# Performance work log

Hardware: AMD Instinct MI355X
Metric: run time of the kernel (lower is better)

The kernel has to match this reference:

```python
import jax, jax.numpy as jnp
import numpy as np

BS, T, IN, HS = 512, 2048, 64, 128


def setup_inputs() -> dict:
    key = jax.random.key(0)
    ks = jax.random.split(key, 6)
    stdv = 1.0 / np.sqrt(HS)
    u = lambda k, shape: jax.random.uniform(k, shape, jnp.float32, -stdv, stdv)
    return {
        "x": jax.random.normal(ks[0], (BS, T, IN), jnp.float32),
        "W": u(ks[1], (IN, 4 * HS)),
        "U": u(ks[2], (HS, 4 * HS)),
        "bias": u(ks[3], (4 * HS,)),
        "linear_w": u(ks[4], (1, HS)),
        "linear_b": u(ks[5], (1,)),
    }


def reference(x, W, U, bias, linear_w, linear_b):
    bs = x.shape[0]
    h0 = jnp.zeros((bs, HS), x.dtype)
    c0 = jnp.zeros((bs, HS), x.dtype)

    def step(carry, x_t):
        h, c = carry
        gates = x_t @ W + h @ U + bias  # [bs, 4*HS]
        i_t = jax.nn.sigmoid(gates[:, :HS])
        f_t = jax.nn.sigmoid(gates[:, HS:2 * HS])
        g_t = jnp.tanh(gates[:, 2 * HS:3 * HS])
        o_t = jax.nn.sigmoid(gates[:, 3 * HS:])
        c = f_t * c + i_t * g_t
        h = o_t * jnp.tanh(c)
        return (h, c), None

    xs = jnp.swapaxes(x, 0, 1)  # [T, bs, IN]
    (h_t, c_t), _ = jax.lax.scan(step, (h0, c0), xs)
    y_t = h_t @ linear_w.T + linear_b  # [bs, 1]
    return (y_t, h_t, c_t)
```

## Files before the change

kernel.cpp:

```cpp
#include <hip/hip_runtime.h>


#define T_STEPS 2048
#define IN_DIM 64
#define HS 128
#define NG 512
#define ROWS 2
#define NBLK 256
#define NTHR 512
#define CH 32
#define NCH (T_STEPS / CH)
#define HROW 144

typedef float f32x4 __attribute__((ext_vector_type(4)));
typedef short s16x8 __attribute__((ext_vector_type(8)));
typedef int   i32x4 __attribute__((ext_vector_type(4)));

__device__ __forceinline__ unsigned f2bf(float f) {
  unsigned u = __float_as_uint(f);
  return (u + 0x7fffu + ((u >> 16) & 1u)) >> 16;
}
__device__ __forceinline__ float bf2f(unsigned short s) {
  return __int_as_float(((int)s) << 16);
}
__device__ __forceinline__ float rcpf(float x) { return __builtin_amdgcn_rcpf(x); }
__device__ __forceinline__ float sigm(float x) { return rcpf(1.f + __expf(-x)); }
__device__ __forceinline__ float tanhfast(float x) {
  return 1.0f - 2.0f * rcpf(__expf(2.0f * x) + 1.0f);
}
__device__ __forceinline__ int xswz(int f) { return f ^ (((f >> 7) & 7) << 3); }

__global__ __launch_bounds__(NTHR, 1)
void lstm_fused(const float* __restrict__ X, const float* __restrict__ W,
                const float* __restrict__ U, const float* __restrict__ B,
                const float* __restrict__ LW, const float* __restrict__ LB,
                float* __restrict__ OUT) {
  __shared__ __align__(16) short Zc[CH * 128 * 8];
  __shared__ __align__(16) float Xl[4096];
  __shared__ __align__(16) unsigned char Hq[2][2][HROW];
  __shared__ float Ys[256];
  __shared__ float Ps[8];

  const int tid  = threadIdx.x;
  const int lane = tid & 63;
  const int w    = tid >> 6;
  const int blk  = blockIdx.x;
  const int lrow = lane & 15;
  const int lg   = lane >> 4;
  const int col8 = (w * 16 + lrow) * 8;

  i32x4 bUq[4][2];
  float scl[4];
  s16x8 bfrW[4][2];
  float biasg[4];
#pragma unroll
  for (int n = 0; n < 4; ++n) {
    const int p = n * HS + w * 16 + lrow;
    float m = 1e-8f;
    for (int k = 0; k < HS; ++k) m = fmaxf(m, fabsf(U[k * NG + p]));
    const float rsu = 127.f / m;
    scl[n] = m / (127.f * 127.f);
#pragma unroll
    for (int kt = 0; kt < 2; ++kt) {
      int vq[4] = {0, 0, 0, 0};
      for (int j = 0; j < 16; ++j) {
        const int k = kt * 64 + (lg << 4) + j;
        int q = (int)rintf(U[k * NG + p] * rsu);
        q = q < -127 ? -127 : (q > 127 ? 127 : q);
        vq[j >> 2] |= (q & 0xff) << ((j & 3) * 8);
      }
      bUq[n][kt] = (i32x4){vq[0], vq[1], vq[2], vq[3]};
    }
#pragma unroll
    for (int kt = 0; kt < 2; ++kt)
#pragma unroll
      for (int j = 0; j < 8; ++j)
        bfrW[n][kt][j] = (short)f2bf(W[(kt * 32 + (lg << 3) + j) * NG + p]);
    biasg[n] = B[p];
  }

  f32x4 sx0, sx1, sx2, sx3;
  auto stage_load = [&](int cc) {
    if (w < 4) {
#pragma unroll
      for (int q = 0; q < 4; ++q) {
        const int f   = w * 1024 + q * 256 + lane * 4;
        const int tlc = f >> 7;
        const int row = (f >> 6) & 1;
        const int k   = f & 63;
        const f32x4 v = *(const f32x4*)(
            X + ((long)(blk * ROWS + row) * T_STEPS + (long)cc * CH + tlc) * IN_DIM + k);
        if (q == 0) sx0 = v; else if (q == 1) sx1 = v;
        else if (q == 2) sx2 = v; else sx3 = v;
      }
    }
  };
  auto stage_write = [&]() {
    if (w < 4) {
#pragma unroll
      for (int q = 0; q < 4; ++q) {
        const int f = w * 1024 + q * 256 + lane * 4;
        const f32x4 v = (q == 0) ? sx0 : (q == 1) ? sx1 : (q == 2) ? sx2 : sx3;
        *(f32x4*)&Xl[xswz(f)] = v;
      }
    }
  };

  stage_load(0);
  stage_write();
  for (int i = tid; i < 2 * 2 * HROW; i += NTHR) ((unsigned char*)Hq)[i] = 0;

  i32x4 afr[2];
  const i32x4 izer = {0, 0, 0, 0};
  afr[0] = izer; afr[1] = izer;

  float creg = 0.f, hreg = 0.f;
  __syncthreads();

#pragma unroll 1
  for (int c = 0; c < NCH; ++c) {
#pragma unroll
    for (int mt = 0; mt < 4; ++mt) {
      const int fb = mt * 1024 + (lrow >> 1) * 128 + (lrow & 1) * 64;
      const int f0 = xswz(fb + 8 * lg);
      const int f1 = xswz(fb + 32 + 8 * lg);
      const f32x4 x0 = *(const f32x4*)&Xl[f0];
      const f32x4 x1 = *(const f32x4*)&Xl[f0 + 4];
      const f32x4 x2 = *(const f32x4*)&Xl[f1];
      const f32x4 x3 = *(const f32x4*)&Xl[f1 + 4];
      s16x8 a0, a1;
#pragma unroll
      for (int j = 0; j < 4; ++j) {
        a0[j] = (short)f2bf(x0[j]); a0[4 + j] = (short)f2bf(x1[j]);
        a1[j] = (short)f2bf(x2[j]); a1[4 + j] = (short)f2bf(x3[j]);
      }
      f32x4 ac[4];
#pragma unroll
      for (int n = 0; n < 4; ++n) {
        ac[n][0] = biasg[n]; ac[n][1] = biasg[n];
        ac[n][2] = biasg[n]; ac[n][3] = biasg[n];
      }
#pragma unroll
      for (int n = 0; n < 4; ++n)
        ac[n] = __builtin_amdgcn_mfma_f32_16x16x32_bf16(a0, bfrW[n][0], ac[n], 0, 0, 0);
#pragma unroll
      for (int n = 0; n < 4; ++n)
        ac[n] = __builtin_amdgcn_mfma_f32_16x16x32_bf16(a1, bfrW[n][1], ac[n], 0, 0, 0);
      s16x8 z0, z1;
#pragma unroll
      for (int n = 0; n < 4; ++n) {
        z0[n] = (short)f2bf(ac[n][0]); z0[4 + n] = (short)f2bf(ac[n][1]);
        z1[n] = (short)f2bf(ac[n][2]); z1[4 + n] = (short)f2bf(ac[n][3]);
      }
      const int tl0 = mt * 8 + 2 * lg;
      *(s16x8*)&Zc[tl0 * 1024 + col8]       = z0;
      *(s16x8*)&Zc[(tl0 + 1) * 1024 + col8] = z1;
    }
    __syncthreads();
    stage_load((c + 1 < NCH) ? c + 1 : c);

#pragma unroll 1
    for (int tl = 0; tl < CH; ++tl) {
      const int t = c * CH + tl;
      const uint2 zu = *(const uint2*)&Zc[tl * 1024 + col8 + (lg & 1) * 4];

      i32x4 acc[4];
#pragma unroll
      for (int n = 0; n < 4; ++n) acc[n] = izer;

      __builtin_amdgcn_s_setprio(1);
#pragma unroll
      for (int kt = 0; kt < 2; ++kt) {
        acc[0] = __builtin_amdgcn_mfma_i32_16x16x64_i8(afr[kt], bUq[0][kt], acc[0], 0, 0, 0);
        acc[1] = __builtin_amdgcn_mfma_i32_16x16x64_i8(afr[kt], bUq[1][kt], acc[1], 0, 0, 0);
        acc[2] = __builtin_amdgcn_mfma_i32_16x16x64_i8(afr[kt], bUq[2][kt], acc[2], 0, 0, 0);
        acc[3] = __builtin_amdgcn_mfma_i32_16x16x64_i8(afr[kt], bUq[3][kt], acc[3], 0, 0, 0);
      }
      __builtin_amdgcn_s_setprio(0);

      if (tl == 4) stage_write();

      if (lane < 32) {
        const float v0 = (float)acc[0][0] * scl[0] + bf2f((unsigned short)(zu.x & 0xffff));
        const float v1 = (float)acc[1][0] * scl[1] + bf2f((unsigned short)(zu.x >> 16));
        const float v2 = (float)acc[2][0] * scl[2] + bf2f((unsigned short)(zu.y & 0xffff));
        const float v3 = (float)acc[3][0] * scl[3] + bf2f((unsigned short)(zu.y >> 16));
        const float iv = sigm(v0), fv = sigm(v1);
        const float gv = tanhfast(v2), ov = sigm(v3);
        creg = fv * creg + iv * gv;
        hreg = ov * tanhfast(creg);
        const int colc = w * 16 + lrow;
        const int r    = lg;
        if (t < T_STEPS - 1) {
          const int hq = (int)rintf(hreg * 127.f);
          Hq[(t + 1) & 1][r][colc] = (unsigned char)hq;
        } else {
          const int row = blk * ROWS + r;
          OUT[512 + row * HS + colc]   = hreg;
          OUT[66048 + row * HS + colc] = creg;
          Ys[r * HS + colc] = LW[colc] * hreg;
        }
      }
      __syncthreads();

      if (t < T_STEPS - 1 && (lrow & 3) == 0 && lrow < 8) {
        const unsigned char* hb = Hq[(t + 1) & 1][lrow >> 2];
        afr[0] = *(const i32x4*)&hb[lg << 4];
        afr[1] = *(const i32x4*)&hb[64 + (lg << 4)];
      }
    }
  }

  if (tid < 8) {
    const int r = tid >> 2, seg = tid & 3;
    float s = 0.f;
#pragma unroll 8
    for (int j = 0; j < 32; ++j) s += Ys[r * 128 + seg * 32 + j];
    Ps[tid] = s;
  }
  __syncthreads();
  if (tid < ROWS) {
    OUT[blk * ROWS + tid] = LB[0] + Ps[tid * 4] + Ps[tid * 4 + 1]
                                  + Ps[tid * 4 + 2] + Ps[tid * 4 + 3];
  }
}

extern "C" void kernel_launch(void* const* d_in, const int* in_sizes, int n_in,
                              void* d_out, int out_size, void* d_ws, size_t ws_size,
                              hipStream_t stream) {
  const float* X  = (const float*)d_in[0];
  const float* W  = (const float*)d_in[1];
  const float* U  = (const float*)d_in[2];
  const float* B  = (const float*)d_in[3];
  const float* LW = (const float*)d_in[4];
  const float* LB = (const float*)d_in[5];
  lstm_fused<<<dim3(NBLK), dim3(NTHR), 0, stream>>>(X, W, U, B, LW, LB, (float*)d_out);
}
```

Measured before the change: 931.1 us.

## Skew two batch rows by half a step to overlap recurrence MFMA with gate math

Splits the two batch rows of each block into separately buffered pipelines, with row B lagging row A by one timestep phase. Row A's gate math now overlaps row B's int8 recurrence MFMAs, and the reverse, so the matrix and vector work of the serial chain can interleave. Each row gets its own h buffer and fragment registers, and an epilogue finishes row B's last step. This adds one more barrier per timestep and more registers in exchange for hiding the latency of the dependent chain.

Measured after the change: 1.699 ms. 1.83x slower.

```diff
diff --git a/kernel.cpp b/kernel.cpp
--- a/kernel.cpp
+++ b/kernel.cpp
@@ -37,7 +37,8 @@
                 float* __restrict__ OUT) {
   __shared__ __align__(16) short Zc[CH * 128 * 8];
   __shared__ __align__(16) float Xl[4096];
-  __shared__ __align__(16) unsigned char Hq[2][2][HROW];
+  __shared__ __align__(16) unsigned char HqA[HROW];
+  __shared__ __align__(16) unsigned char HqB[HROW];
   __shared__ float Ys[256];
   __shared__ float Ps[8];
 
@@ -108,12 +109,13 @@
 
   stage_load(0);
   stage_write();
-  for (int i = tid; i < 2 * 2 * HROW; i += NTHR) ((unsigned char*)Hq)[i] = 0;
-
-  i32x4 afr[2];
+  for (int i = tid; i < HROW; i += NTHR) { HqA[i] = 0; HqB[i] = 0; }
+
   const i32x4 izer = {0, 0, 0, 0};
-  afr[0] = izer; afr[1] = izer;
-
+  i32x4 afrA[2] = {izer, izer};
+  i32x4 afrB[2] = {izer, izer};
+  i32x4 accB[4] = {izer, izer, izer, izer};
+  uint2 zuB = {0u, 0u};
   float creg = 0.f, hreg = 0.f;
   __syncthreads();
 
@@ -164,52 +166,96 @@
       const int t = c * CH + tl;
       const uint2 zu = *(const uint2*)&Zc[tl * 1024 + col8 + (lg & 1) * 4];
 
-      i32x4 acc[4];
-#pragma unroll
-      for (int n = 0; n < 4; ++n) acc[n] = izer;
-
+      if (t > 0 && lg == 1) {
+        const float v0 = (float)accB[0][0] * scl[0] + bf2f((unsigned short)(zuB.x & 0xffff));
+        const float v1 = (float)accB[1][0] * scl[1] + bf2f((unsigned short)(zuB.x >> 16));
+        const float v2 = (float)accB[2][0] * scl[2] + bf2f((unsigned short)(zuB.y & 0xffff));
+        const float v3 = (float)accB[3][0] * scl[3] + bf2f((unsigned short)(zuB.y >> 16));
+        const float iv = sigm(v0), fv = sigm(v1);
+        const float gv = tanhfast(v2), ov = sigm(v3);
+        creg = fv * creg + iv * gv;
+        hreg = ov * tanhfast(creg);
+        HqB[w * 16 + lrow] = (unsigned char)(int)rintf(hreg * 127.f);
+      }
+      zuB = zu;
+
+      i32x4 accA[4] = {izer, izer, izer, izer};
       __builtin_amdgcn_s_setprio(1);
 #pragma unroll
       for (int kt = 0; kt < 2; ++kt) {
-        acc[0] = __builtin_amdgcn_mfma_i32_16x16x64_i8(afr[kt], bUq[0][kt], acc[0], 0, 0, 0);
-        acc[1] = __builtin_amdgcn_mfma_i32_16x16x64_i8(afr[kt], bUq[1][kt], acc[1], 0, 0, 0);
-        acc[2] = __builtin_amdgcn_mfma_i32_16x16x64_i8(afr[kt], bUq[2][kt], acc[2], 0, 0, 0);
-        acc[3] = __builtin_amdgcn_mfma_i32_16x16x64_i8(afr[kt], bUq[3][kt], acc[3], 0, 0, 0);
+        accA[0] = __builtin_amdgcn_mfma_i32_16x16x64_i8(afrA[kt], bUq[0][kt], accA[0], 0, 0, 0);
+        accA[1] = __builtin_amdgcn_mfma_i32_16x16x64_i8(afrA[kt], bUq[1][kt], accA[1], 0, 0, 0);
+        accA[2] = __builtin_amdgcn_mfma_i32_16x16x64_i8(afrA[kt], bUq[2][kt], accA[2], 0, 0, 0);
+        accA[3] = __builtin_amdgcn_mfma_i32_16x16x64_i8(afrA[kt], bUq[3][kt], accA[3], 0, 0, 0);
       }
       __builtin_amdgcn_s_setprio(0);
-
-      if (tl == 4) stage_write();
-
-      if (lane < 32) {
-        const float v0 = (float)acc[0][0] * scl[0] + bf2f((unsigned short)(zu.x & 0xffff));
-        const float v1 = (float)acc[1][0] * scl[1] + bf2f((unsigned short)(zu.x >> 16));
-        const float v2 = (float)acc[2][0] * scl[2] + bf2f((unsigned short)(zu.y & 0xffff));
-        const float v3 = (float)acc[3][0] * scl[3] + bf2f((unsigned short)(zu.y >> 16));
+      __syncthreads();
+
+      if (lrow == 4) {
+        afrB[0] = *(const i32x4*)&HqB[lg << 4];
+        afrB[1] = *(const i32x4*)&HqB[64 + (lg << 4)];
+      }
+
+      if (lg == 0) {
+        const float v0 = (float)accA[0][0] * scl[0] + bf2f((unsigned short)(zu.x & 0xffff));
+        const float v1 = (float)accA[1][0] * scl[1] + bf2f((unsigned short)(zu.x >> 16));
+        const float v2 = (float)accA[2][0] * scl[2] + bf2f((unsigned short)(zu.y & 0xffff));
+        const float v3 = (float)accA[3][0] * scl[3] + bf2f((unsigned short)(zu.y >> 16));
         const float iv = sigm(v0), fv = sigm(v1);
         const float gv = tanhfast(v2), ov = sigm(v3);
         creg = fv * creg + iv * gv;
         hreg = ov * tanhfast(creg);
         const int colc = w * 16 + lrow;
-        const int r    = lg;
         if (t < T_STEPS - 1) {
-          const int hq = (int)rintf(hreg * 127.f);
-          Hq[(t + 1) & 1][r][colc] = (unsigned char)hq;
+          HqA[colc] = (unsigned char)(int)rintf(hreg * 127.f);
         } else {
-          const int row = blk * ROWS + r;
+          const int row = blk * ROWS;
           OUT[512 + row * HS + colc]   = hreg;
           OUT[66048 + row * HS + colc] = creg;
-          Ys[r * HS + colc] = LW[colc] * hreg;
+          Ys[colc] = LW[colc] * hreg;
         }
       }
+
+      __builtin_amdgcn_s_setprio(1);
+#pragma unroll
+      for (int kt = 0; kt < 2; ++kt) {
+        accB[0] = (kt == 0) ? __builtin_amdgcn_mfma_i32_16x16x64_i8(afrB[0], bUq[0][0], izer, 0, 0, 0)
+                            : __builtin_amdgcn_mfma_i32_16x16x64_i8(afrB[1], bUq[0][1], accB[0], 0, 0, 0);
+        accB[1] = (kt == 0) ? __builtin_amdgcn_mfma_i32_16x16x64_i8(afrB[0], bUq[1][0], izer, 0, 0, 0)
+                            : __builtin_amdgcn_mfma_i32_16x16x64_i8(afrB[1], bUq[1][1], accB[1], 0, 0, 0);
+        accB[2] = (kt == 0) ? __builtin_amdgcn_mfma_i32_16x16x64_i8(afrB[0], bUq[2][0], izer, 0, 0, 0)
+                            : __builtin_amdgcn_mfma_i32_16x16x64_i8(afrB[1], bUq[2][1], accB[2], 0, 0, 0);
+        accB[3] = (kt == 0) ? __builtin_amdgcn_mfma_i32_16x16x64_i8(afrB[0], bUq[3][0], izer, 0, 0, 0)
+                            : __builtin_amdgcn_mfma_i32_16x16x64_i8(afrB[1], bUq[3][1], accB[3], 0, 0, 0);
+      }
+      __builtin_amdgcn_s_setprio(0);
+
+      if (tl == 4) stage_write();
       __syncthreads();
 
-      if (t < T_STEPS - 1 && (lrow & 3) == 0 && lrow < 8) {
-        const unsigned char* hb = Hq[(t + 1) & 1][lrow >> 2];
-        afr[0] = *(const i32x4*)&hb[lg << 4];
-        afr[1] = *(const i32x4*)&hb[64 + (lg << 4)];
-      }
-    }
-  }
+      if (t < T_STEPS - 1 && lrow == 0) {
+        afrA[0] = *(const i32x4*)&HqA[lg << 4];
+        afrA[1] = *(const i32x4*)&HqA[64 + (lg << 4)];
+      }
+    }
+  }
+
+  if (lg == 1) {
+    const float v0 = (float)accB[0][0] * scl[0] + bf2f((unsigned short)(zuB.x & 0xffff));
+    const float v1 = (float)accB[1][0] * scl[1] + bf2f((unsigned short)(zuB.x >> 16));
+    const float v2 = (float)accB[2][0] * scl[2] + bf2f((unsigned short)(zuB.y & 0xffff));
+    const float v3 = (float)accB[3][0] * scl[3] + bf2f((unsigned short)(zuB.y >> 16));
+    const float iv = sigm(v0), fv = sigm(v1);
+    const float gv = tanhfast(v2), ov = sigm(v3);
+    creg = fv * creg + iv * gv;
+    hreg = ov * tanhfast(creg);
+    const int colc = w * 16 + lrow;
+    const int row  = blk * ROWS + 1;
+    OUT[512 + row * HS + colc]   = hreg;
+    OUT[66048 + row * HS + colc] = creg;
+    Ys[HS + colc] = LW[colc] * hreg;
+  }
+  __syncthreads();
 
   if (tid < 8) {
     const int r = tid >> 2, seg = tid & 3;
```
